# Performance work log

Measured on AMD Instinct MI355X. Metric: run time of the kernel, lower is better.

The kernel has to match this reference:

```python
import jax, jax.numpy as jnp
import numpy as np

N_NODES = 50000
N_EDGES = 800000
NODE_DIM = 64
EDGE_DIM = 64
ALPHA = 2.0
EPS = 1e-5
NEG_SLOPE = 0.2


def setup_inputs() -> dict:
    key = jax.random.key(0)
    ks = jax.random.split(key, 16)
    s = 0.1  # keep params small for numerical sanity
    inp = {
        "V": jax.random.normal(ks[0], (N_NODES, NODE_DIM), jnp.float32),
        "E": jax.random.normal(ks[1], (N_EDGES, EDGE_DIM), jnp.float32),
        "src": jax.random.randint(ks[2], (N_EDGES,), 0, N_NODES),
        "dst": jax.random.randint(ks[3], (N_EDGES,), 0, N_NODES),
        # GenMessage.A: 2-layer MLP edge_dim -> edge_dim
        "mlp_w1": jax.random.normal(ks[4], (EDGE_DIM, EDGE_DIM), jnp.float32) * s,
        "mlp_b1": jnp.zeros((EDGE_DIM,), jnp.float32),
        "mlp_w2": jax.random.normal(ks[5], (EDGE_DIM, EDGE_DIM), jnp.float32) * s,
        "mlp_b2": jnp.zeros((EDGE_DIM,), jnp.float32),
        # GenMessage.B (gate) and .C (shift): edge_dim -> node_dim
        "Bw": jax.random.normal(ks[6], (EDGE_DIM, NODE_DIM), jnp.float32) * s,
        "Bb": jnp.zeros((NODE_DIM,), jnp.float32),
        "Cw": jax.random.normal(ks[7], (EDGE_DIM, NODE_DIM), jnp.float32) * s,
        "Cb": jnp.zeros((NODE_DIM,), jnp.float32),
        # NodePooling: two node_dim -> node_dim linears
        "pAw": jax.random.normal(ks[8], (NODE_DIM, NODE_DIM), jnp.float32) * s,
        "pAb": jnp.zeros((NODE_DIM,), jnp.float32),
        "pBw": jax.random.normal(ks[9], (NODE_DIM, NODE_DIM), jnp.float32) * s,
        "pBb": jnp.zeros((NODE_DIM,), jnp.float32),
    }
    return inp


def reference(V, E, src, dst, mlp_w1, mlp_b1, mlp_w2, mlp_b2,
              Bw, Bb, Cw, Cb, pAw, pAb, pBw, pBb):
    n = V.shape[0]
    # V = act(V)
    V = jax.nn.leaky_relu(V, NEG_SLOPE)
    # NodePooling: Lin -> LeakyReLU -> Lin
    Vp = jax.nn.leaky_relu(V @ pAw + pAb, NEG_SLOPE) @ pBw + pBb
    # GenMessage: edge MLP, gate + shift
    x = jax.nn.relu(E @ mlp_w1 + mlp_b1)
    x = jax.nn.relu(x @ mlp_w2 + mlp_b2)
    scale = jax.nn.sigmoid(x @ Bw + Bb)   # [Ne, node_dim]
    shift = x @ Cw + Cb
    msg = scale * Vp[src] + shift         # gather src node features
    M = jnp.power(jnp.clip(msg, EPS, None), ALPHA)
    # mean aggregation onto dst nodes
    ssum = jax.ops.segment_sum(M, dst, num_segments=n)
    cnt = jax.ops.segment_sum(jnp.ones((M.shape[0],), M.dtype), dst, num_segments=n)
    mean = ssum / jnp.maximum(cnt, 1.0)[:, None]
    return jnp.power(mean, 1.0 / ALPHA)
```

## Files before the change

### kernel.cpp

```cpp
#include <hip/hip_runtime.h>
#include <hip/hip_bf16.h>
#include <math.h>

#define N_NODES 50000
#define N_EDGES 800000
#define DIM 64
#define NEG_SLOPE 0.2f
#define EPS 1e-5f

typedef __attribute__((ext_vector_type(8))) short short8v;
typedef __attribute__((ext_vector_type(4))) float f32x4;

__device__ __forceinline__ float lrelu(float v) { return fmaxf(v, NEG_SLOPE * v); }

__device__ __forceinline__ unsigned short bfbits(float v) {
    return __bfloat16_as_ushort(__float2bfloat16(v));
}
__device__ __forceinline__ unsigned pack2bf(float a, float b) {
    union { __hip_bfloat162 h; unsigned u; } cvt;
    cvt.h = __float22bfloat162_rn(make_float2(a, b));
    return cvt.u;
}

__device__ __forceinline__ unsigned swz(unsigned row, unsigned byteInRow) {
    return row * 128u + (byteInRow ^ ((row & 7u) << 4));
}

#define LDS_BUF 16384

#define WFRAG_ENTRIES 512

#define SCANA_BLOCKS 49

__global__ __launch_bounds__(256) void prep_kernel(
    const float* __restrict__ w1, const float* __restrict__ w2,
    const float* __restrict__ Bw, const float* __restrict__ Cw,
    const float* __restrict__ pAw, const float* __restrict__ pBw,
    unsigned short* __restrict__ wbf, int* __restrict__ cnt)
{
    const int t = threadIdx.x;
    if (blockIdx.x >= 6) {
        const int idx = (blockIdx.x - 6) * 1024 + t * 4;
        if (idx + 3 < N_NODES) {
            int4 z = {0, 0, 0, 0};
            *(int4*)(cnt + idx) = z;
        } else {
#pragma unroll
            for (int i = 0; i < 4; ++i)
                if (idx + i < N_NODES) cnt[idx + i] = 0;
        }
        return;
    }
    const float* W;
    switch (blockIdx.x) {
        case 0: W = w1; break;
        case 1: W = w2; break;
        case 2: W = Bw; break;
        case 3: W = Cw; break;
        case 4: W = pAw; break;
        default: W = pBw; break;
    }
#pragma unroll
    for (int ii = 0; ii < 2; ++ii) {
        const int idx = t * 2 + ii;
        const int ks  = idx >> 8;
        const int g   = (idx >> 6) & 3;
        const int col = idx & 63;
        unsigned short* o = wbf + (size_t)blockIdx.x * 4096 + (size_t)idx * 8;
#pragma unroll
        for (int j = 0; j < 8; ++j)
            o[j] = bfbits(W[(32 * ks + 8 * g + j) * DIM + col]);
    }
}

__device__ __forceinline__ short8v wfrag(const unsigned short* wbf, int m, int ks,
                                         int g, int col) {
    return ((const short8v*)wbf)[m * WFRAG_ENTRIES + (ks * 4 + g) * 64 + col];
}

__global__ __launch_bounds__(256) void node_kernel(
    const float* __restrict__ V,
    const unsigned short* __restrict__ wbf,
    const float* __restrict__ pAb, const float* __restrict__ pBb,
    float* __restrict__ Vp)
{
    __shared__ __align__(16) unsigned char sm[2 * LDS_BUF];
    unsigned char* bufA = sm;
    unsigned char* bufB = sm + LDS_BUF;

    const int t    = threadIdx.x;
    const int w    = t >> 6;
    const int lane = t & 63;
    const int g    = lane >> 4;
    const int c    = lane & 15;
    const int col  = 16 * w + c;
    const unsigned colbyte = (unsigned)col * 2;
    const int base = blockIdx.x * 128;

    {
        const int row = t >> 1;
        const int n = base + row;
        if (n < N_NODES) {
            const float4* Vr = (const float4*)(V + (size_t)n * DIM + (t & 1) * 32);
#pragma unroll
            for (int ci = 0; ci < 4; ++ci) {
                float4 qa = Vr[2 * ci];
                float4 qb = Vr[2 * ci + 1];
                uint4 u;
                u.x = pack2bf(lrelu(qa.x), lrelu(qa.y));
                u.y = pack2bf(lrelu(qa.z), lrelu(qa.w));
                u.z = pack2bf(lrelu(qb.x), lrelu(qb.y));
                u.w = pack2bf(lrelu(qb.z), lrelu(qb.w));
                *(uint4*)(bufA + swz(row, (t & 1) * 64 + 16 * ci)) = u;
            }
        } else {
            uint4 z = {0u, 0u, 0u, 0u};
#pragma unroll
            for (int ci = 0; ci < 4; ++ci)
                *(uint4*)(bufA + swz(row, (t & 1) * 64 + 16 * ci)) = z;
        }
    }

    const short8v af0 = wfrag(wbf, 4, 0, g, col), af1 = wfrag(wbf, 4, 1, g, col);
    const short8v bf0 = wfrag(wbf, 5, 0, g, col), bf1 = wfrag(wbf, 5, 1, g, col);
    const float bbA = pAb[col], bbB = pBb[col];

    __syncthreads();

#pragma unroll
    for (int mt = 0; mt < 8; ++mt) {
        const int arow = mt * 16 + c;
        short8v a0 = *(const short8v*)(bufA + swz(arow, 16 * g));
        short8v a1 = *(const short8v*)(bufA + swz(arow, 64 + 16 * g));
        f32x4 acc = {0.f, 0.f, 0.f, 0.f};
        acc = __builtin_amdgcn_mfma_f32_16x16x32_bf16(a0, af0, acc, 0, 0, 0);
        acc = __builtin_amdgcn_mfma_f32_16x16x32_bf16(a1, af1, acc, 0, 0, 0);
#pragma unroll
        for (int r = 0; r < 4; ++r) {
            const float v = lrelu(acc[r] + bbA);
            *(unsigned short*)(bufB + swz(mt * 16 + 4 * g + r, colbyte)) = bfbits(v);
        }
    }
    __syncthreads();

#pragma unroll
    for (int mt = 0; mt < 8; ++mt) {
        const int arow = mt * 16 + c;
        short8v a0 = *(const short8v*)(bufB + swz(arow, 16 * g));
        short8v a1 = *(const short8v*)(bufB + swz(arow, 64 + 16 * g));
        f32x4 acc = {0.f, 0.f, 0.f, 0.f};
        acc = __builtin_amdgcn_mfma_f32_16x16x32_bf16(a0, bf0, acc, 0, 0, 0);
        acc = __builtin_amdgcn_mfma_f32_16x16x32_bf16(a1, bf1, acc, 0, 0, 0);
#pragma unroll
        for (int r = 0; r < 4; ++r) {
            const int n = base + mt * 16 + 4 * g + r;
            if (n < N_NODES) Vp[(size_t)n * DIM + col] = acc[r] + bbB;
        }
    }
}

__global__ __launch_bounds__(256) void hist_kernel(
    const int* __restrict__ dst, int* __restrict__ cnt, int* __restrict__ rank)
{
    const int e = blockIdx.x * 256 + threadIdx.x;
    rank[e] = atomicAdd(&cnt[dst[e]], 1);
}

__global__ __launch_bounds__(256) void scanA_kernel(
    const int* __restrict__ cnt, int* __restrict__ lofs, int* __restrict__ btot)
{
    __shared__ int ts[256];
    const int t = threadIdx.x;
    const int nb = blockIdx.x * 1024 + t * 4;
    int4 c = {0, 0, 0, 0};
    if (nb + 3 < N_NODES) {
        c = *(const int4*)(cnt + nb);
    } else {
        if (nb + 0 < N_NODES) c.x = cnt[nb + 0];
        if (nb + 1 < N_NODES) c.y = cnt[nb + 1];
        if (nb + 2 < N_NODES) c.z = cnt[nb + 2];
        if (nb + 3 < N_NODES) c.w = cnt[nb + 3];
    }
    ts[t] = c.x + c.y + c.z + c.w;
    __syncthreads();
    for (int off = 1; off < 256; off <<= 1) {
        const int add = (t >= off) ? ts[t - off] : 0;
        __syncthreads();
        ts[t] += add;
        __syncthreads();
    }
    int4 o;
    o.x = (t == 0) ? 0 : ts[t - 1];
    o.y = o.x + c.x;
    o.z = o.y + c.y;
    o.w = o.z + c.z;
    if (nb + 3 < N_NODES) {
        *(int4*)(lofs + nb) = o;
    } else {
        if (nb + 0 < N_NODES) lofs[nb + 0] = o.x;
        if (nb + 1 < N_NODES) lofs[nb + 1] = o.y;
        if (nb + 2 < N_NODES) lofs[nb + 2] = o.z;
        if (nb + 3 < N_NODES) lofs[nb + 3] = o.w;
    }
    if (t == 255) btot[blockIdx.x] = ts[255];
}

__global__ __launch_bounds__(64) void scanB_kernel(
    const int* __restrict__ btot, int* __restrict__ bbase)
{
    const int t = threadIdx.x;
    const int own = (t < SCANA_BLOCKS) ? btot[t] : 0;
    int v = own;
    for (int off = 1; off < 64; off <<= 1) {
        const int u = __shfl_up(v, off, 64);
        if (t >= off) v += u;
    }
    if (t < SCANA_BLOCKS) bbase[t] = v - own;
}

__global__ __launch_bounds__(256) void edge_kernel(
    const float* __restrict__ E,
    const int* __restrict__ src, const int* __restrict__ dst,
    const int* __restrict__ rank,
    const int* __restrict__ lofs, const int* __restrict__ bbase,
    const unsigned short* __restrict__ wbf,
    const float* __restrict__ b1, const float* __restrict__ b2,
    const float* __restrict__ Bb, const float* __restrict__ Cb,
    const float* __restrict__ Vp,
    __hip_bfloat16* __restrict__ msg)
{
    __shared__ __align__(16) unsigned char sm[2 * LDS_BUF];
    unsigned char* bufA = sm;
    unsigned char* bufB = sm + LDS_BUF;

    const int t    = threadIdx.x;
    const int w    = t >> 6;
    const int lane = t & 63;
    const int g    = lane >> 4;
    const int c    = lane & 15;
    const int col  = 16 * w + c;
    const unsigned colbyte = (unsigned)col * 2;
    const int base = blockIdx.x * 128;

    const int myrow = t >> 1;
    const int d_my = dst[base + myrow];
    const int pos = lofs[d_my] + bbase[d_my >> 10] + rank[base + myrow];

    float vpre[32];
#pragma unroll
    for (int mt = 0; mt < 8; ++mt) {
#pragma unroll
        for (int r = 0; r < 4; ++r) {
            const int sv = src[base + mt * 16 + 4 * g + r];
            vpre[mt * 4 + r] = Vp[(size_t)sv * DIM + col];
        }
    }

    {
        const float4* Ep = (const float4*)(E + (size_t)(base + myrow) * DIM + (t & 1) * 32);
#pragma unroll
        for (int ci = 0; ci < 4; ++ci) {
            float4 qa = Ep[2 * ci];
            float4 qb = Ep[2 * ci + 1];
            uint4 u;
            u.x = pack2bf(qa.x, qa.y); u.y = pack2bf(qa.z, qa.w);
            u.z = pack2bf(qb.x, qb.y); u.w = pack2bf(qb.z, qb.w);
            *(uint4*)(bufA + swz(myrow, (t & 1) * 64 + 16 * ci)) = u;
        }
    }

    const short8v w1f0 = wfrag(wbf, 0, 0, g, col), w1f1 = wfrag(wbf, 0, 1, g, col);
    const short8v w2f0 = wfrag(wbf, 1, 0, g, col), w2f1 = wfrag(wbf, 1, 1, g, col);
    const short8v bwf0 = wfrag(wbf, 2, 0, g, col), bwf1 = wfrag(wbf, 2, 1, g, col);
    const short8v cwf0 = wfrag(wbf, 3, 0, g, col), cwf1 = wfrag(wbf, 3, 1, g, col);
    const float bb1 = b1[col], bb2 = b2[col], bbB = Bb[col], bbC = Cb[col];

    __syncthreads();

#pragma unroll
    for (int mt = 0; mt < 8; ++mt) {
        const int arow = mt * 16 + c;
        short8v a0 = *(const short8v*)(bufA + swz(arow, 16 * g));
        short8v a1 = *(const short8v*)(bufA + swz(arow, 64 + 16 * g));
        f32x4 acc = {0.f, 0.f, 0.f, 0.f};
        acc = __builtin_amdgcn_mfma_f32_16x16x32_bf16(a0, w1f0, acc, 0, 0, 0);
        acc = __builtin_amdgcn_mfma_f32_16x16x32_bf16(a1, w1f1, acc, 0, 0, 0);
#pragma unroll
        for (int r = 0; r < 4; ++r) {
            const float v = fmaxf(acc[r] + bb1, 0.f);
            *(unsigned short*)(bufB + swz(mt * 16 + 4 * g + r, colbyte)) = bfbits(v);
        }
    }
    __syncthreads();

#pragma unroll
    for (int mt = 0; mt < 8; ++mt) {
        const int arow = mt * 16 + c;
        short8v a0 = *(const short8v*)(bufB + swz(arow, 16 * g));
        short8v a1 = *(const short8v*)(bufB + swz(arow, 64 + 16 * g));
        f32x4 acc = {0.f, 0.f, 0.f, 0.f};
        acc = __builtin_amdgcn_mfma_f32_16x16x32_bf16(a0, w2f0, acc, 0, 0, 0);
        acc = __builtin_amdgcn_mfma_f32_16x16x32_bf16(a1, w2f1, acc, 0, 0, 0);
#pragma unroll
        for (int r = 0; r < 4; ++r) {
            const float v = fmaxf(acc[r] + bb2, 0.f);
            *(unsigned short*)(bufA + swz(mt * 16 + 4 * g + r, colbyte)) = bfbits(v);
        }
    }
    __syncthreads();

#pragma unroll
    for (int mt = 0; mt < 8; ++mt) {
        const int arow = mt * 16 + c;
        short8v a0 = *(const short8v*)(bufA + swz(arow, 16 * g));
        short8v a1 = *(const short8v*)(bufA + swz(arow, 64 + 16 * g));
        f32x4 t0 = {0.f, 0.f, 0.f, 0.f};
        t0 = __builtin_amdgcn_mfma_f32_16x16x32_bf16(a0, bwf0, t0, 0, 0, 0);
        t0 = __builtin_amdgcn_mfma_f32_16x16x32_bf16(a1, bwf1, t0, 0, 0, 0);
        f32x4 t1 = {0.f, 0.f, 0.f, 0.f};
        t1 = __builtin_amdgcn_mfma_f32_16x16x32_bf16(a0, cwf0, t1, 0, 0, 0);
        t1 = __builtin_amdgcn_mfma_f32_16x16x32_bf16(a1, cwf1, t1, 0, 0, 0);
#pragma unroll
        for (int r = 0; r < 4; ++r) {
            const float gate = 1.f / (1.f + __expf(-(t0[r] + bbB)));
            const float sh = t1[r] + bbC;
            float m = fmaf(gate, vpre[mt * 4 + r], sh);
            m = fmaxf(m, EPS);
            m = m * m;
            *(unsigned short*)(bufB + swz(mt * 16 + 4 * g + r, colbyte)) = bfbits(m);
        }
    }
    __syncthreads();

    {
        uint4 v[4];
#pragma unroll
        for (int ci = 0; ci < 4; ++ci)
            v[ci] = *(const uint4*)(bufB + swz(myrow, (t & 1) * 64 + 16 * ci));
        uint4* dp = (uint4*)((unsigned short*)msg + (size_t)pos * DIM + (t & 1) * 32);
#pragma unroll
        for (int ci = 0; ci < 4; ++ci) dp[ci] = v[ci];
    }
}

__global__ __launch_bounds__(256) void aggregate_kernel(
    const __hip_bfloat16* __restrict__ msg,
    const int* __restrict__ lofs, const int* __restrict__ bbase,
    const int* __restrict__ cnt,
    float* __restrict__ out)
{
    const int n = (blockIdx.x * 256 + threadIdx.x) >> 6;
    const int lane = threadIdx.x & 63;
    if (n >= N_NODES) return;
    const int start = lofs[n] + bbase[n >> 10];
    const int deg = cnt[n];
    const int rowg = lane >> 3;
    const int dblk = lane & 7;

    const unsigned short* bp = (const unsigned short*)msg + (size_t)start * DIM + dblk * 8;
    float acc0 = 0.f, acc1 = 0.f, acc2 = 0.f, acc3 = 0.f;
    float acc4 = 0.f, acc5 = 0.f, acc6 = 0.f, acc7 = 0.f;
    for (int i = 0; i < deg; i += 8) {
        const int r = i + rowg;
        if (r < deg) {
            const uint4 u = *(const uint4*)(bp + (size_t)r * DIM);
            acc0 += __uint_as_float(u.x << 16);
            acc1 += __uint_as_float(u.x & 0xffff0000u);
            acc2 += __uint_as_float(u.y << 16);
            acc3 += __uint_as_float(u.y & 0xffff0000u);
            acc4 += __uint_as_float(u.z << 16);
            acc5 += __uint_as_float(u.z & 0xffff0000u);
            acc6 += __uint_as_float(u.w << 16);
            acc7 += __uint_as_float(u.w & 0xffff0000u);
        }
    }
#pragma unroll
    for (int m = 8; m <= 32; m <<= 1) {
        acc0 += __shfl_xor(acc0, m, 64);
        acc1 += __shfl_xor(acc1, m, 64);
        acc2 += __shfl_xor(acc2, m, 64);
        acc3 += __shfl_xor(acc3, m, 64);
        acc4 += __shfl_xor(acc4, m, 64);
        acc5 += __shfl_xor(acc5, m, 64);
        acc6 += __shfl_xor(acc6, m, 64);
        acc7 += __shfl_xor(acc7, m, 64);
    }
    if (rowg == 0) {
        const float dinv = (deg > 0) ? 1.0f / (float)deg : 0.0f;
        float4 o0, o1;
        o0.x = sqrtf(acc0 * dinv); o0.y = sqrtf(acc1 * dinv);
        o0.z = sqrtf(acc2 * dinv); o0.w = sqrtf(acc3 * dinv);
        o1.x = sqrtf(acc4 * dinv); o1.y = sqrtf(acc5 * dinv);
        o1.z = sqrtf(acc6 * dinv); o1.w = sqrtf(acc7 * dinv);
        float4* op = (float4*)(out + (size_t)n * DIM + dblk * 8);
        op[0] = o0;
        op[1] = o1;
    }
}

extern "C" void kernel_launch(void* const* d_in, const int* in_sizes, int n_in,
                              void* d_out, int out_size, void* d_ws, size_t ws_size,
                              hipStream_t stream) {
    const float* V   = (const float*)d_in[0];
    const float* E   = (const float*)d_in[1];
    const int*   src = (const int*)d_in[2];
    const int*   dst = (const int*)d_in[3];
    const float* w1  = (const float*)d_in[4];
    const float* b1  = (const float*)d_in[5];
    const float* w2  = (const float*)d_in[6];
    const float* b2  = (const float*)d_in[7];
    const float* Bw  = (const float*)d_in[8];
    const float* Bb  = (const float*)d_in[9];
    const float* Cw  = (const float*)d_in[10];
    const float* Cb  = (const float*)d_in[11];
    const float* pAw = (const float*)d_in[12];
    const float* pAb = (const float*)d_in[13];
    const float* pBw = (const float*)d_in[14];
    const float* pBb = (const float*)d_in[15];

    float* out = (float*)d_out;

    char* p = (char*)d_ws;
    float* Vp = (float*)p;                    p += (size_t)N_NODES * DIM * sizeof(float);
    __hip_bfloat16* msg = (__hip_bfloat16*)p; p += (size_t)N_EDGES * DIM * 2;
    int* cnt  = (int*)p; p += (size_t)50176 * 4;
    int* lofs = (int*)p; p += (size_t)50176 * 4;
    int* rank = (int*)p; p += (size_t)N_EDGES * 4;
    unsigned short* wbf = (unsigned short*)p; p += (size_t)6 * 4096 * 2;
    int* btot  = (int*)p; p += (size_t)64 * 4;
    int* bbase = (int*)p; p += (size_t)64 * 4;

    prep_kernel<<<6 + SCANA_BLOCKS, 256, 0, stream>>>(w1, w2, Bw, Cw, pAw, pBw, wbf, cnt);
    hist_kernel<<<N_EDGES / 256, 256, 0, stream>>>(dst, cnt, rank);
    node_kernel<<<(N_NODES + 127) / 128, 256, 0, stream>>>(V, wbf, pAb, pBb, Vp);
    scanA_kernel<<<SCANA_BLOCKS, 256, 0, stream>>>(cnt, lofs, btot);
    scanB_kernel<<<1, 64, 0, stream>>>(btot, bbase);
    edge_kernel<<<N_EDGES / 128, 256, 0, stream>>>(E, src, dst, rank, lofs, bbase, wbf,
                                                   b1, b2, Bb, Cb, Vp, msg);
    aggregate_kernel<<<(N_NODES * 64 + 255) / 256, 256, 0, stream>>>(msg, lofs, bbase, cnt, out);
}
```

Before: 196.0 us.

## Give each wave its own 32 edge rows to remove block barriers in edge MLP

Edge rows are now split across waves: each wave owns 32 edges and computes all 64 output columns with transposed MFMAs (weights as A operand, activations as B). The wave reads only LDS rows it wrote itself, so all __syncthreads between the GEMM phases are removed. Outputs are stored packed as uint2 per row, and the Vp gather becomes float4 loads per source row. In exchange, every wave reloads all weight fragments and biases inside the loop instead of holding a single column slice, which adds global/L1 traffic and register pressure.

New measurement: 216.7 us. 10.5% more time.

```diff
diff --git a/kernel.cpp b/kernel.cpp
--- a/kernel.cpp
+++ b/kernel.cpp
@@ -234,30 +234,32 @@
     unsigned char* bufB = sm + LDS_BUF;
 
     const int t    = threadIdx.x;
-    const int w    = t >> 6;
     const int lane = t & 63;
+    const int wv   = t >> 6;
+    const int c    = lane & 15;
     const int g    = lane >> 4;
-    const int c    = lane & 15;
-    const int col  = 16 * w + c;
-    const unsigned colbyte = (unsigned)col * 2;
+    const int wrow = wv * 32;
     const int base = blockIdx.x * 128;
 
-    const int myrow = t >> 1;
-    const int d_my = dst[base + myrow];
-    const int pos = lofs[d_my] + bbase[d_my >> 10] + rank[base + myrow];
-
-    float vpre[32];
-#pragma unroll
-    for (int mt = 0; mt < 8; ++mt) {
-#pragma unroll
-        for (int r = 0; r < 4; ++r) {
-            const int sv = src[base + mt * 16 + 4 * g + r];
-            vpre[mt * 4 + r] = Vp[(size_t)sv * DIM + col];
-        }
+    const int e0g = base + wrow + c;
+    const int s0  = src[e0g];
+    const int s1  = src[e0g + 16];
+
+    const int lr = lane >> 1;
+    const int h  = lane & 1;
+    const int gedge = base + wrow + lr;
+    const int d_my  = dst[gedge];
+    const int pos   = lofs[d_my] + bbase[d_my >> 10] + rank[gedge];
+
+    float4 vpre0[4], vpre1[4];
+#pragma unroll
+    for (int m = 0; m < 4; ++m) {
+        vpre0[m] = *(const float4*)(Vp + (size_t)s0 * DIM + 16 * m + 4 * g);
+        vpre1[m] = *(const float4*)(Vp + (size_t)s1 * DIM + 16 * m + 4 * g);
     }
 
     {
-        const float4* Ep = (const float4*)(E + (size_t)(base + myrow) * DIM + (t & 1) * 32);
+        const float4* Ep = (const float4*)(E + (size_t)gedge * DIM + h * 32);
 #pragma unroll
         for (int ci = 0; ci < 4; ++ci) {
             float4 qa = Ep[2 * ci];
@@ -265,79 +267,91 @@
             uint4 u;
             u.x = pack2bf(qa.x, qa.y); u.y = pack2bf(qa.z, qa.w);
             u.z = pack2bf(qb.x, qb.y); u.w = pack2bf(qb.z, qb.w);
-            *(uint4*)(bufA + swz(myrow, (t & 1) * 64 + 16 * ci)) = u;
-        }
-    }
-
-    const short8v w1f0 = wfrag(wbf, 0, 0, g, col), w1f1 = wfrag(wbf, 0, 1, g, col);
-    const short8v w2f0 = wfrag(wbf, 1, 0, g, col), w2f1 = wfrag(wbf, 1, 1, g, col);
-    const short8v bwf0 = wfrag(wbf, 2, 0, g, col), bwf1 = wfrag(wbf, 2, 1, g, col);
-    const short8v cwf0 = wfrag(wbf, 3, 0, g, col), cwf1 = wfrag(wbf, 3, 1, g, col);
-    const float bb1 = b1[col], bb2 = b2[col], bbB = Bb[col], bbC = Cb[col];
-
-    __syncthreads();
-
-#pragma unroll
-    for (int mt = 0; mt < 8; ++mt) {
-        const int arow = mt * 16 + c;
-        short8v a0 = *(const short8v*)(bufA + swz(arow, 16 * g));
-        short8v a1 = *(const short8v*)(bufA + swz(arow, 64 + 16 * g));
-        f32x4 acc = {0.f, 0.f, 0.f, 0.f};
-        acc = __builtin_amdgcn_mfma_f32_16x16x32_bf16(a0, w1f0, acc, 0, 0, 0);
-        acc = __builtin_amdgcn_mfma_f32_16x16x32_bf16(a1, w1f1, acc, 0, 0, 0);
-#pragma unroll
-        for (int r = 0; r < 4; ++r) {
-            const float v = fmaxf(acc[r] + bb1, 0.f);
-            *(unsigned short*)(bufB + swz(mt * 16 + 4 * g + r, colbyte)) = bfbits(v);
-        }
-    }
-    __syncthreads();
-
-#pragma unroll
-    for (int mt = 0; mt < 8; ++mt) {
-        const int arow = mt * 16 + c;
-        short8v a0 = *(const short8v*)(bufB + swz(arow, 16 * g));
-        short8v a1 = *(const short8v*)(bufB + swz(arow, 64 + 16 * g));
-        f32x4 acc = {0.f, 0.f, 0.f, 0.f};
-        acc = __builtin_amdgcn_mfma_f32_16x16x32_bf16(a0, w2f0, acc, 0, 0, 0);
-        acc = __builtin_amdgcn_mfma_f32_16x16x32_bf16(a1, w2f1, acc, 0, 0, 0);
-#pragma unroll
-        for (int r = 0; r < 4; ++r) {
-            const float v = fmaxf(acc[r] + bb2, 0.f);
-            *(unsigned short*)(bufA + swz(mt * 16 + 4 * g + r, colbyte)) = bfbits(v);
-        }
-    }
-    __syncthreads();
-
-#pragma unroll
-    for (int mt = 0; mt < 8; ++mt) {
-        const int arow = mt * 16 + c;
-        short8v a0 = *(const short8v*)(bufA + swz(arow, 16 * g));
-        short8v a1 = *(const short8v*)(bufA + swz(arow, 64 + 16 * g));
-        f32x4 t0 = {0.f, 0.f, 0.f, 0.f};
-        t0 = __builtin_amdgcn_mfma_f32_16x16x32_bf16(a0, bwf0, t0, 0, 0, 0);
-        t0 = __builtin_amdgcn_mfma_f32_16x16x32_bf16(a1, bwf1, t0, 0, 0, 0);
-        f32x4 t1 = {0.f, 0.f, 0.f, 0.f};
-        t1 = __builtin_amdgcn_mfma_f32_16x16x32_bf16(a0, cwf0, t1, 0, 0, 0);
-        t1 = __builtin_amdgcn_mfma_f32_16x16x32_bf16(a1, cwf1, t1, 0, 0, 0);
-#pragma unroll
-        for (int r = 0; r < 4; ++r) {
-            const float gate = 1.f / (1.f + __expf(-(t0[r] + bbB)));
-            const float sh = t1[r] + bbC;
-            float m = fmaf(gate, vpre[mt * 4 + r], sh);
-            m = fmaxf(m, EPS);
-            m = m * m;
-            *(unsigned short*)(bufB + swz(mt * 16 + 4 * g + r, colbyte)) = bfbits(m);
-        }
-    }
-    __syncthreads();
+            *(uint4*)(bufA + swz(wrow + lr, h * 64 + 16 * ci)) = u;
+        }
+    }
+
+#define GEMM_PHASE(BIN, BOUT, MAT, BIASP)                                        \
+    {                                                                            \
+        const short8v xf00 = *(const short8v*)(BIN + swz(wrow + c,      16 * g)); \
+        const short8v xf01 = *(const short8v*)(BIN + swz(wrow + c,      64 + 16 * g)); \
+        const short8v xf10 = *(const short8v*)(BIN + swz(wrow + 16 + c, 16 * g)); \
+        const short8v xf11 = *(const short8v*)(BIN + swz(wrow + 16 + c, 64 + 16 * g)); \
+        _Pragma("unroll")                                                        \
+        for (int m = 0; m < 4; ++m) {                                            \
+            const short8v a0 = wfrag(wbf, MAT, 0, g, 16 * m + c);                \
+            const short8v a1 = wfrag(wbf, MAT, 1, g, 16 * m + c);                \
+            const float4 bias = *(const float4*)(BIASP + 16 * m + 4 * g);        \
+            f32x4 acc0 = {0.f, 0.f, 0.f, 0.f};                                   \
+            acc0 = __builtin_amdgcn_mfma_f32_16x16x32_bf16(a0, xf00, acc0, 0, 0, 0); \
+            acc0 = __builtin_amdgcn_mfma_f32_16x16x32_bf16(a1, xf01, acc0, 0, 0, 0); \
+            f32x4 acc1 = {0.f, 0.f, 0.f, 0.f};                                   \
+            acc1 = __builtin_amdgcn_mfma_f32_16x16x32_bf16(a0, xf10, acc1, 0, 0, 0); \
+            acc1 = __builtin_amdgcn_mfma_f32_16x16x32_bf16(a1, xf11, acc1, 0, 0, 0); \
+            uint2 p0, p1;                                                        \
+            p0.x = pack2bf(fmaxf(acc0[0] + bias.x, 0.f), fmaxf(acc0[1] + bias.y, 0.f)); \
+            p0.y = pack2bf(fmaxf(acc0[2] + bias.z, 0.f), fmaxf(acc0[3] + bias.w, 0.f)); \
+            p1.x = pack2bf(fmaxf(acc1[0] + bias.x, 0.f), fmaxf(acc1[1] + bias.y, 0.f)); \
+            p1.y = pack2bf(fmaxf(acc1[2] + bias.z, 0.f), fmaxf(acc1[3] + bias.w, 0.f)); \
+            *(uint2*)(BOUT + swz(wrow + c,      32 * m + 8 * g)) = p0;           \
+            *(uint2*)(BOUT + swz(wrow + 16 + c, 32 * m + 8 * g)) = p1;           \
+        }                                                                        \
+    }
+
+    GEMM_PHASE(bufA, bufB, 0, b1);
+    GEMM_PHASE(bufB, bufA, 1, b2);
+#undef GEMM_PHASE
+
+    {
+        const short8v xf00 = *(const short8v*)(bufA + swz(wrow + c,      16 * g));
+        const short8v xf01 = *(const short8v*)(bufA + swz(wrow + c,      64 + 16 * g));
+        const short8v xf10 = *(const short8v*)(bufA + swz(wrow + 16 + c, 16 * g));
+        const short8v xf11 = *(const short8v*)(bufA + swz(wrow + 16 + c, 64 + 16 * g));
+#pragma unroll
+        for (int m = 0; m < 4; ++m) {
+            const short8v a0B = wfrag(wbf, 2, 0, g, 16 * m + c);
+            const short8v a1B = wfrag(wbf, 2, 1, g, 16 * m + c);
+            const short8v a0C = wfrag(wbf, 3, 0, g, 16 * m + c);
+            const short8v a1C = wfrag(wbf, 3, 1, g, 16 * m + c);
+            const float4 biasB = *(const float4*)(Bb + 16 * m + 4 * g);
+            const float4 biasC = *(const float4*)(Cb + 16 * m + 4 * g);
+            f32x4 gb0 = {0.f, 0.f, 0.f, 0.f}, gb1 = {0.f, 0.f, 0.f, 0.f};
+            gb0 = __builtin_amdgcn_mfma_f32_16x16x32_bf16(a0B, xf00, gb0, 0, 0, 0);
+            gb0 = __builtin_amdgcn_mfma_f32_16x16x32_bf16(a1B, xf01, gb0, 0, 0, 0);
+            gb1 = __builtin_amdgcn_mfma_f32_16x16x32_bf16(a0B, xf10, gb1, 0, 0, 0);
+            gb1 = __builtin_amdgcn_mfma_f32_16x16x32_bf16(a1B, xf11, gb1, 0, 0, 0);
+            f32x4 sc0 = {0.f, 0.f, 0.f, 0.f}, sc1 = {0.f, 0.f, 0.f, 0.f};
+            sc0 = __builtin_amdgcn_mfma_f32_16x16x32_bf16(a0C, xf00, sc0, 0, 0, 0);
+            sc0 = __builtin_amdgcn_mfma_f32_16x16x32_bf16(a1C, xf01, sc0, 0, 0, 0);
+            sc1 = __builtin_amdgcn_mfma_f32_16x16x32_bf16(a0C, xf10, sc1, 0, 0, 0);
+            sc1 = __builtin_amdgcn_mfma_f32_16x16x32_bf16(a1C, xf11, sc1, 0, 0, 0);
+
+            float m0[4], m1[4];
+#pragma unroll
+            for (int r = 0; r < 4; ++r) {
+                const float bB = (r == 0) ? biasB.x : (r == 1) ? biasB.y : (r == 2) ? biasB.z : biasB.w;
+                const float bC = (r == 0) ? biasC.x : (r == 1) ? biasC.y : (r == 2) ? biasC.z : biasC.w;
+                const float v0 = (r == 0) ? vpre0[m].x : (r == 1) ? vpre0[m].y : (r == 2) ? vpre0[m].z : vpre0[m].w;
+                const float v1 = (r == 0) ? vpre1[m].x : (r == 1) ? vpre1[m].y : (r == 2) ? vpre1[m].z : vpre1[m].w;
+                const float g0 = 1.f / (1.f + __expf(-(gb0[r] + bB)));
+                const float g1 = 1.f / (1.f + __expf(-(gb1[r] + bB)));
+                float q0 = fmaf(g0, v0, sc0[r] + bC); q0 = fmaxf(q0, EPS); m0[r] = q0 * q0;
+                float q1 = fmaf(g1, v1, sc1[r] + bC); q1 = fmaxf(q1, EPS); m1[r] = q1 * q1;
+            }
+            uint2 p0, p1;
+            p0.x = pack2bf(m0[0], m0[1]); p0.y = pack2bf(m0[2], m0[3]);
+            p1.x = pack2bf(m1[0], m1[1]); p1.y = pack2bf(m1[2], m1[3]);
+            *(uint2*)(bufB + swz(wrow + c,      32 * m + 8 * g)) = p0;
+            *(uint2*)(bufB + swz(wrow + 16 + c, 32 * m + 8 * g)) = p1;
+        }
+    }
 
     {
         uint4 v[4];
 #pragma unroll
         for (int ci = 0; ci < 4; ++ci)
-            v[ci] = *(const uint4*)(bufB + swz(myrow, (t & 1) * 64 + 16 * ci));
-        uint4* dp = (uint4*)((unsigned short*)msg + (size_t)pos * DIM + (t & 1) * 32);
+            v[ci] = *(const uint4*)(bufB + swz(wrow + lr, h * 64 + 16 * ci));
+        uint4* dp = (uint4*)((unsigned short*)msg + (size_t)pos * DIM + h * 32);
 #pragma unroll
         for (int ci = 0; ci < 4; ++ci) dp[ci] = v[ci];
     }
```

## Keep edge MLP activations in registers via transposed MFMA, dropping LDS staging

Applied to the files above, without the earlier changes.

Computes the edge MLP transposed (weights as the A operand, edge features as B) so each MFMA's output fragment directly forms the next layer's input fragment in registers. This removes all shared-memory staging and block barriers. Weight matrices 1-3 are stored in a permuted K order to match that register layout. Each wave now handles 16 edges instead of 32, so the grid doubles, and weight fragments are reloaded from global/L2 per m-tile rather than held once. Output writes become 8-byte scattered stores instead of 16-byte row writes.

New measurement: 247.8 us. +26.4%, slower.

```diff
diff --git a/kernel.cpp b/kernel.cpp
--- a/kernel.cpp
+++ b/kernel.cpp
@@ -10,6 +10,8 @@
 
 typedef __attribute__((ext_vector_type(8))) short short8v;
 typedef __attribute__((ext_vector_type(4))) float f32x4;
+
+union frag_u { unsigned u[8]; short8v v[2]; };
 
 __device__ __forceinline__ float lrelu(float v) { return fmaxf(v, NEG_SLOPE * v); }
 
@@ -60,6 +62,7 @@
         case 4: W = pAw; break;
         default: W = pBw; break;
     }
+    const bool permuted = (blockIdx.x >= 1 && blockIdx.x <= 3);
 #pragma unroll
     for (int ii = 0; ii < 2; ++ii) {
         const int idx = t * 2 + ii;
@@ -68,8 +71,11 @@
         const int col = idx & 63;
         unsigned short* o = wbf + (size_t)blockIdx.x * 4096 + (size_t)idx * 8;
 #pragma unroll
-        for (int j = 0; j < 8; ++j)
-            o[j] = bfbits(W[(32 * ks + 8 * g + j) * DIM + col]);
+        for (int j = 0; j < 8; ++j) {
+            const int k = permuted ? (16 * (2 * ks + (j >> 2)) + 4 * g + (j & 3))
+                                   : (32 * ks + 8 * g + j);
+            o[j] = bfbits(W[k * DIM + col]);
+        }
     }
 }
 
@@ -229,117 +235,88 @@
     const float* __restrict__ Vp,
     __hip_bfloat16* __restrict__ msg)
 {
-    __shared__ __align__(16) unsigned char sm[2 * LDS_BUF];
-    unsigned char* bufA = sm;
-    unsigned char* bufB = sm + LDS_BUF;
-
     const int t    = threadIdx.x;
-    const int w    = t >> 6;
     const int lane = t & 63;
-    const int g    = lane >> 4;
     const int c    = lane & 15;
-    const int col  = 16 * w + c;
-    const unsigned colbyte = (unsigned)col * 2;
-    const int base = blockIdx.x * 128;
-
-    const int myrow = t >> 1;
-    const int d_my = dst[base + myrow];
-    const int pos = lofs[d_my] + bbase[d_my >> 10] + rank[base + myrow];
-
-    float vpre[32];
-#pragma unroll
-    for (int mt = 0; mt < 8; ++mt) {
+    const int hi   = lane >> 4;
+    const int e    = blockIdx.x * 64 + (t >> 6) * 16 + c;
+
+    const int d_my = dst[e];
+    const int s0   = src[e];
+    const int pos  = lofs[d_my] + bbase[d_my >> 10] + rank[e];
+
+    float4 vpre[4];
+#pragma unroll
+    for (int m = 0; m < 4; ++m)
+        vpre[m] = *(const float4*)(Vp + (size_t)s0 * DIM + 16 * m + 4 * hi);
+
+    short8v xb0, xb1;
+    {
+        const float* Ep = E + (size_t)e * DIM + 8 * hi;
+        const float4 qa = *(const float4*)(Ep + 0);
+        const float4 qb = *(const float4*)(Ep + 4);
+        const float4 qc = *(const float4*)(Ep + 32);
+        const float4 qd = *(const float4*)(Ep + 36);
+        frag_u f;
+        f.u[0] = pack2bf(qa.x, qa.y); f.u[1] = pack2bf(qa.z, qa.w);
+        f.u[2] = pack2bf(qb.x, qb.y); f.u[3] = pack2bf(qb.z, qb.w);
+        f.u[4] = pack2bf(qc.x, qc.y); f.u[5] = pack2bf(qc.z, qc.w);
+        f.u[6] = pack2bf(qd.x, qd.y); f.u[7] = pack2bf(qd.z, qd.w);
+        xb0 = f.v[0]; xb1 = f.v[1];
+    }
+
+#define PHASE(MAT, BIASP)                                                         \
+    {                                                                             \
+        frag_u nx;                                                                \
+        _Pragma("unroll")                                                         \
+        for (int m = 0; m < 4; ++m) {                                             \
+            const short8v a0 = wfrag(wbf, MAT, 0, hi, 16 * m + c);                \
+            const short8v a1 = wfrag(wbf, MAT, 1, hi, 16 * m + c);                \
+            f32x4 acc = {0.f, 0.f, 0.f, 0.f};                                     \
+            acc = __builtin_amdgcn_mfma_f32_16x16x32_bf16(a0, xb0, acc, 0, 0, 0); \
+            acc = __builtin_amdgcn_mfma_f32_16x16x32_bf16(a1, xb1, acc, 0, 0, 0); \
+            const float4 bias = *(const float4*)(BIASP + 16 * m + 4 * hi);        \
+            nx.u[2 * m]     = pack2bf(fmaxf(acc[0] + bias.x, 0.f),                \
+                                      fmaxf(acc[1] + bias.y, 0.f));               \
+            nx.u[2 * m + 1] = pack2bf(fmaxf(acc[2] + bias.z, 0.f),                \
+                                      fmaxf(acc[3] + bias.w, 0.f));               \
+        }                                                                         \
+        xb0 = nx.v[0]; xb1 = nx.v[1];                                             \
+    }
+
+    PHASE(0, b1);
+    PHASE(1, b2);
+#undef PHASE
+
+#pragma unroll
+    for (int m = 0; m < 4; ++m) {
+        const short8v a0B = wfrag(wbf, 2, 0, hi, 16 * m + c);
+        const short8v a1B = wfrag(wbf, 2, 1, hi, 16 * m + c);
+        const short8v a0C = wfrag(wbf, 3, 0, hi, 16 * m + c);
+        const short8v a1C = wfrag(wbf, 3, 1, hi, 16 * m + c);
+        f32x4 gb = {0.f, 0.f, 0.f, 0.f};
+        gb = __builtin_amdgcn_mfma_f32_16x16x32_bf16(a0B, xb0, gb, 0, 0, 0);
+        gb = __builtin_amdgcn_mfma_f32_16x16x32_bf16(a1B, xb1, gb, 0, 0, 0);
+        f32x4 sc = {0.f, 0.f, 0.f, 0.f};
+        sc = __builtin_amdgcn_mfma_f32_16x16x32_bf16(a0C, xb0, sc, 0, 0, 0);
+        sc = __builtin_amdgcn_mfma_f32_16x16x32_bf16(a1C, xb1, sc, 0, 0, 0);
+        const float4 biasB = *(const float4*)(Bb + 16 * m + 4 * hi);
+        const float4 biasC = *(const float4*)(Cb + 16 * m + 4 * hi);
+        const float* vp = (const float*)&vpre[m];
+        const float* bBp = (const float*)&biasB;
+        const float* bCp = (const float*)&biasC;
+        float mm[4];
 #pragma unroll
         for (int r = 0; r < 4; ++r) {
-            const int sv = src[base + mt * 16 + 4 * g + r];
-            vpre[mt * 4 + r] = Vp[(size_t)sv * DIM + col];
-        }
-    }
-
-    {
-        const float4* Ep = (const float4*)(E + (size_t)(base + myrow) * DIM + (t & 1) * 32);
-#pragma unroll
-        for (int ci = 0; ci < 4; ++ci) {
-            float4 qa = Ep[2 * ci];
-            float4 qb = Ep[2 * ci + 1];
-            uint4 u;
-            u.x = pack2bf(qa.x, qa.y); u.y = pack2bf(qa.z, qa.w);
-            u.z = pack2bf(qb.x, qb.y); u.w = pack2bf(qb.z, qb.w);
-            *(uint4*)(bufA + swz(myrow, (t & 1) * 64 + 16 * ci)) = u;
-        }
-    }
-
-    const short8v w1f0 = wfrag(wbf, 0, 0, g, col), w1f1 = wfrag(wbf, 0, 1, g, col);
-    const short8v w2f0 = wfrag(wbf, 1, 0, g, col), w2f1 = wfrag(wbf, 1, 1, g, col);
-    const short8v bwf0 = wfrag(wbf, 2, 0, g, col), bwf1 = wfrag(wbf, 2, 1, g, col);
-    const short8v cwf0 = wfrag(wbf, 3, 0, g, col), cwf1 = wfrag(wbf, 3, 1, g, col);
-    const float bb1 = b1[col], bb2 = b2[col], bbB = Bb[col], bbC = Cb[col];
-
-    __syncthreads();
-
-#pragma unroll
-    for (int mt = 0; mt < 8; ++mt) {
-        const int arow = mt * 16 + c;
-        short8v a0 = *(const short8v*)(bufA + swz(arow, 16 * g));
-        short8v a1 = *(const short8v*)(bufA + swz(arow, 64 + 16 * g));
-        f32x4 acc = {0.f, 0.f, 0.f, 0.f};
-        acc = __builtin_amdgcn_mfma_f32_16x16x32_bf16(a0, w1f0, acc, 0, 0, 0);
-        acc = __builtin_amdgcn_mfma_f32_16x16x32_bf16(a1, w1f1, acc, 0, 0, 0);
-#pragma unroll
-        for (int r = 0; r < 4; ++r) {
-            const float v = fmaxf(acc[r] + bb1, 0.f);
-            *(unsigned short*)(bufB + swz(mt * 16 + 4 * g + r, colbyte)) = bfbits(v);
-        }
-    }
-    __syncthreads();
-
-#pragma unroll
-    for (int mt = 0; mt < 8; ++mt) {
-        const int arow = mt * 16 + c;
-        short8v a0 = *(const short8v*)(bufB + swz(arow, 16 * g));
-        short8v a1 = *(const short8v*)(bufB + swz(arow, 64 + 16 * g));
-        f32x4 acc = {0.f, 0.f, 0.f, 0.f};
-        acc = __builtin_amdgcn_mfma_f32_16x16x32_bf16(a0, w2f0, acc, 0, 0, 0);
-        acc = __builtin_amdgcn_mfma_f32_16x16x32_bf16(a1, w2f1, acc, 0, 0, 0);
-#pragma unroll
-        for (int r = 0; r < 4; ++r) {
-            const float v = fmaxf(acc[r] + bb2, 0.f);
-            *(unsigned short*)(bufA + swz(mt * 16 + 4 * g + r, colbyte)) = bfbits(v);
-        }
-    }
-    __syncthreads();
-
-#pragma unroll
-    for (int mt = 0; mt < 8; ++mt) {
-        const int arow = mt * 16 + c;
-        short8v a0 = *(const short8v*)(bufA + swz(arow, 16 * g));
-        short8v a1 = *(const short8v*)(bufA + swz(arow, 64 + 16 * g));
-        f32x4 t0 = {0.f, 0.f, 0.f, 0.f};
-        t0 = __builtin_amdgcn_mfma_f32_16x16x32_bf16(a0, bwf0, t0, 0, 0, 0);
-        t0 = __builtin_amdgcn_mfma_f32_16x16x32_bf16(a1, bwf1, t0, 0, 0, 0);
-        f32x4 t1 = {0.f, 0.f, 0.f, 0.f};
-        t1 = __builtin_amdgcn_mfma_f32_16x16x32_bf16(a0, cwf0, t1, 0, 0, 0);
-        t1 = __builtin_amdgcn_mfma_f32_16x16x32_bf16(a1, cwf1, t1, 0, 0, 0);
-#pragma unroll
-        for (int r = 0; r < 4; ++r) {
-            const float gate = 1.f / (1.f + __expf(-(t0[r] + bbB)));
-            const float sh = t1[r] + bbC;
-            float m = fmaf(gate, vpre[mt * 4 + r], sh);
-            m = fmaxf(m, EPS);
-            m = m * m;
-            *(unsigned short*)(bufB + swz(mt * 16 + 4 * g + r, colbyte)) = bfbits(m);
-        }
-    }
-    __syncthreads();
-
-    {
-        uint4 v[4];
-#pragma unroll
-        for (int ci = 0; ci < 4; ++ci)
-            v[ci] = *(const uint4*)(bufB + swz(myrow, (t & 1) * 64 + 16 * ci));
-        uint4* dp = (uint4*)((unsigned short*)msg + (size_t)pos * DIM + (t & 1) * 32);
-#pragma unroll
-        for (int ci = 0; ci < 4; ++ci) dp[ci] = v[ci];
+            const float gate = 1.f / (1.f + __expf(-(gb[r] + bBp[r])));
+            float q = fmaf(gate, vp[r], sc[r] + bCp[r]);
+            q = fmaxf(q, EPS);
+            mm[r] = q * q;
+        }
+        uint2 p;
+        p.x = pack2bf(mm[0], mm[1]);
+        p.y = pack2bf(mm[2], mm[3]);
+        *(uint2*)((unsigned short*)msg + (size_t)pos * DIM + 16 * m + 4 * hi) = p;
     }
 }
 
@@ -435,7 +412,7 @@
     node_kernel<<<(N_NODES + 127) / 128, 256, 0, stream>>>(V, wbf, pAb, pBb, Vp);
     scanA_kernel<<<SCANA_BLOCKS, 256, 0, stream>>>(cnt, lofs, btot);
     scanB_kernel<<<1, 64, 0, stream>>>(btot, bbase);
-    edge_kernel<<<N_EDGES / 128, 256, 0, stream>>>(E, src, dst, rank, lofs, bbase, wbf,
-                                                   b1, b2, Bb, Cb, Vp, msg);
+    edge_kernel<<<N_EDGES / 64, 256, 0, stream>>>(E, src, dst, rank, lofs, bbase, wbf,
+                                                  b1, b2, Bb, Cb, Vp, msg);
     aggregate_kernel<<<(N_NODES * 64 + 255) / 256, 256, 0, stream>>>(msg, lofs, bbase, cnt, out);
 }
```
